# Optimization experiments

Hardware: AMD Instinct MI355X
Metric: run time of the kernel (lower is better)

## Reference

```python
import jax, jax.numpy as jnp
import numpy as np

B, T, E, H = 2, 2048, 768, 12
D = E // H  # head_dim = 64
EPS = 1e-5


def layer_norm(x, scale, shift):
    mean = x.mean(axis=-1, keepdims=True)
    # torch .var() default is unbiased (ddof=1)
    var = x.var(axis=-1, keepdims=True, ddof=1)
    return scale * (x - mean) / jnp.sqrt(var + EPS) + shift


def gelu(x):
    c = jnp.sqrt(jnp.asarray(2.0 / jnp.pi, dtype=x.dtype))
    return 0.5 * x * (1.0 + jnp.tanh(c * (x + 0.044715 * x * x * x)))


def setup_inputs() -> dict:
    key = jax.random.key(0)
    ks = jax.random.split(key, 12)
    s = 0.02
    return {
        "x": jax.random.normal(ks[0], (B, T, E), jnp.float32),
        "wq": jax.random.normal(ks[1], (E, E), jnp.float32) * s,
        "wk": jax.random.normal(ks[2], (E, E), jnp.float32) * s,
        "wv": jax.random.normal(ks[3], (E, E), jnp.float32) * s,
        "wo": jax.random.normal(ks[4], (E, E), jnp.float32) * s,
        "bo": jnp.zeros((E,), jnp.float32),
        "ln1_scale": jnp.ones((E,), jnp.float32),
        "ln1_shift": jnp.zeros((E,), jnp.float32),
        "ln2_scale": jnp.ones((E,), jnp.float32),
        "ln2_shift": jnp.zeros((E,), jnp.float32),
        "w1": jax.random.normal(ks[5], (E, 4 * E), jnp.float32) * s,
        "b1": jnp.zeros((4 * E,), jnp.float32),
        "w2": jax.random.normal(ks[6], (4 * E, E), jnp.float32) * s,
        "b2": jnp.zeros((E,), jnp.float32),
    }


def reference(x, wq, wk, wv, wo, bo, ln1_scale, ln1_shift, ln2_scale, ln2_shift,
              w1, b1, w2, b2):
    b, t, e = x.shape
    resid = x
    h = layer_norm(x, ln1_scale, ln1_shift)
    # qkv projections (no bias), split heads -> [b, H, t, D]
    q = (h @ wq).reshape(b, t, H, D).transpose(0, 2, 1, 3)
    k = (h @ wk).reshape(b, t, H, D).transpose(0, 2, 1, 3)
    v = (h @ wv).reshape(b, t, H, D).transpose(0, 2, 1, 3)
    scores = jnp.einsum("bhqd,bhkd->bhqk", q, k) / jnp.sqrt(jnp.asarray(D, x.dtype))
    causal = jnp.tril(jnp.ones((t, t), bool))
    scores = jnp.where(causal[None, None], scores, -jnp.inf)
    attn = jax.nn.softmax(scores, axis=-1)  # dropout p=0 (eval)
    ctx = jnp.einsum("bhqk,bhkd->bhqd", attn, v)
    ctx = ctx.transpose(0, 2, 1, 3).reshape(b, t, e)
    h = ctx @ wo + bo
    x = h + resid

    resid = x
    h = layer_norm(x, ln2_scale, ln2_shift)
    h = gelu(h @ w1 + b1) @ w2 + b2
    return h + resid
```

## Files before the change

### kernel.cpp

```cpp
#include <hip/hip_runtime.h>
#include <hip/hip_bf16.h>
#include <math.h>

typedef __bf16 bf16_t;
typedef __bf16 bf16x4 __attribute__((ext_vector_type(4)));
typedef __bf16 bf16x8 __attribute__((ext_vector_type(8)));
typedef float f32x4 __attribute__((ext_vector_type(4)));

#define TB 2048
#define BB 2
#define EE 768
#define HH 12
#define MM (BB * TB)
#define E3 (3 * EE)
#define E4 (4 * EE)

#define GLL16(g, l)                                                        \
  __builtin_amdgcn_global_load_lds(                                       \
      (const __attribute__((address_space(1))) void*)(g),                 \
      (__attribute__((address_space(3))) void*)(l), 16, 0, 0)

__global__ __launch_bounds__(256) void k_transpose_w(const float* __restrict__ w,
                                                     bf16_t* __restrict__ wT,
                                                     int K, int N) {
  __shared__ bf16_t tile[64][72];
  int kt = blockIdx.x * 64, nt = blockIdx.y * 64;
  int tid = threadIdx.x;
  int r = tid >> 2, c = (tid & 3) * 16;
  const float* src = w + (size_t)(kt + r) * N + nt + c;
  bf16x8 t0, t1;
#pragma unroll
  for (int j = 0; j < 8; j++) { t0[j] = (bf16_t)src[j]; t1[j] = (bf16_t)src[8 + j]; }
  *(bf16x8*)&tile[r][c] = t0;
  *(bf16x8*)&tile[r][c + 8] = t1;
  __syncthreads();
  bf16_t* dst = wT + (size_t)(nt + r) * K + kt + c;
  bf16x8 o0, o1;
#pragma unroll
  for (int j = 0; j < 8; j++) { o0[j] = tile[c + j][r]; o1[j] = tile[c + 8 + j][r]; }
  *(bf16x8*)dst = o0;
  *(bf16x8*)(dst + 8) = o1;
}

__global__ __launch_bounds__(256) void k_transpose_v(const bf16_t* __restrict__ qkv,
                                                     bf16_t* __restrict__ vt) {
  __shared__ bf16_t tile[64][72];
  int tt = blockIdx.x;
  int bh = blockIdx.y;
  int b = bh / HH, h = bh - b * HH;
  int tid = threadIdx.x;
  int r = tid >> 2, c = (tid & 3) * 16;
  const bf16_t* src = qkv + (size_t)(b * TB + tt * 64 + r) * E3 + 2 * EE + h * 64 + c;
  *(bf16x8*)&tile[r][c] = *(const bf16x8*)src;
  *(bf16x8*)&tile[r][c + 8] = *(const bf16x8*)(src + 8);
  __syncthreads();
  bf16_t* dst = vt + ((size_t)bh * 64 + r) * TB + tt * 64 + c;
  bf16x8 o0, o1;
#pragma unroll
  for (int j = 0; j < 8; j++) { o0[j] = tile[c + j][r]; o1[j] = tile[c + 8 + j][r]; }
  *(bf16x8*)dst = o0;
  *(bf16x8*)(dst + 8) = o1;
}

__global__ __launch_bounds__(256) void k_layernorm_bf16(
    const float* __restrict__ x, const float* __restrict__ sc,
    const float* __restrict__ sh, bf16_t* __restrict__ out) {
  int wave = threadIdx.x >> 6, lane = threadIdx.x & 63;
  int row = blockIdx.x * 4 + wave;
  const float* xr = x + (size_t)row * EE;
  float v[12];
  float s = 0.f, sq = 0.f;
#pragma unroll
  for (int i = 0; i < 12; i++) {
    float t = xr[lane + 64 * i];
    v[i] = t; s += t; sq += t * t;
  }
#pragma unroll
  for (int off = 1; off < 64; off <<= 1) {
    s += __shfl_xor(s, off);
    sq += __shfl_xor(sq, off);
  }
  float mean = s * (1.f / EE);
  float var = (sq - (float)EE * mean * mean) * (1.f / (EE - 1));
  float rstd = rsqrtf(var + 1e-5f);
  bf16_t* orow = out + (size_t)row * EE;
#pragma unroll
  for (int i = 0; i < 12; i++) {
    int e = lane + 64 * i;
    orow[e] = (bf16_t)(sc[e] * (v[i] - mean) * rstd + sh[e]);
  }
}

__global__ __launch_bounds__(256) void k_gemm128(
    const bf16_t* __restrict__ A, const bf16_t* __restrict__ Bt,
    int M, int N, int K, int kLen, int epi,
    float* __restrict__ outf, bf16_t* __restrict__ outb,
    const float* __restrict__ bias, const float* __restrict__ resid) {
  __shared__ bf16_t As[128 * 32];
  __shared__ bf16_t Bs[128 * 32];
  int tid = threadIdx.x;
  int wave = tid >> 6, lane = tid & 63;
  int m0 = blockIdx.y * 128, n0 = blockIdx.x * 128;
  int kOff = blockIdx.z * kLen;
  int wm = (wave >> 1) * 64, wn = (wave & 1) * 64;
  int lm = lane & 15, quad = lane >> 4;

  int srow = wave * 32 + (lane >> 2);
  int scol = (lane & 3) * 8;
  const bf16_t* Ap0 = A + (size_t)(m0 + srow) * K + kOff + scol;
  const bf16_t* Ap1 = A + (size_t)(m0 + srow + 16) * K + kOff + scol;
  const bf16_t* Bp0 = Bt + (size_t)(n0 + srow) * K + kOff + scol;
  const bf16_t* Bp1 = Bt + (size_t)(n0 + srow + 16) * K + kOff + scol;
  bf16_t* ldsA0 = &As[(wave * 32) * 32];
  bf16_t* ldsA1 = &As[(wave * 32 + 16) * 32];
  bf16_t* ldsB0 = &Bs[(wave * 32) * 32];
  bf16_t* ldsB1 = &Bs[(wave * 32 + 16) * 32];

  f32x4 acc[4][4];
#pragma unroll
  for (int i = 0; i < 4; i++)
#pragma unroll
    for (int j = 0; j < 4; j++) acc[i][j] = (f32x4){0.f, 0.f, 0.f, 0.f};

  for (int k0 = 0; k0 < kLen; k0 += 32) {
    __syncthreads();
    GLL16(Ap0 + k0, ldsA0);
    GLL16(Ap1 + k0, ldsA1);
    GLL16(Bp0 + k0, ldsB0);
    GLL16(Bp1 + k0, ldsB1);
    __syncthreads();
    bf16x8 af[4], bfr[4];
#pragma unroll
    for (int i = 0; i < 4; i++)
      af[i] = *(const bf16x8*)&As[(wm + i * 16 + lm) * 32 + quad * 8];
#pragma unroll
    for (int j = 0; j < 4; j++)
      bfr[j] = *(const bf16x8*)&Bs[(wn + j * 16 + lm) * 32 + quad * 8];
#pragma unroll
    for (int i = 0; i < 4; i++)
#pragma unroll
      for (int j = 0; j < 4; j++)
        acc[i][j] = __builtin_amdgcn_mfma_f32_16x16x32_bf16(af[i], bfr[j], acc[i][j], 0, 0, 0);
  }

  size_t pbase = (size_t)blockIdx.z * M * N;
#pragma unroll
  for (int i = 0; i < 4; i++) {
#pragma unroll
    for (int j = 0; j < 4; j++) {
      int col = n0 + wn + j * 16 + lm;
#pragma unroll
      for (int r = 0; r < 4; r++) {
        int row = m0 + wm + i * 16 + quad * 4 + r;
        size_t o = (size_t)row * N + col;
        float c = acc[i][j][r];
        if (epi == 0) {
          outb[o] = (bf16_t)c;
        } else if (epi == 1) {
          float xg = c + bias[col];
          float u = 0.7978845608028654f * (xg + 0.044715f * xg * xg * xg);
          float t = 1.f - 2.f / (__expf(2.f * u) + 1.f);
          outb[o] = (bf16_t)(0.5f * xg * (1.f + t));
        } else if (epi == 2) {
          outf[o] = c + bias[col] + resid[o];
        } else {
          outb[pbase + o] = (bf16_t)c;
        }
      }
    }
  }
}

__global__ __launch_bounds__(256) void k_reduce_ln2(
    const bf16_t* __restrict__ p, const float* __restrict__ bo_,
    const float* __restrict__ x, const float* __restrict__ sc,
    const float* __restrict__ sh, float* __restrict__ x1,
    bf16_t* __restrict__ h2) {
  int wave = threadIdx.x >> 6, lane = threadIdx.x & 63;
  int row = blockIdx.x * 4 + wave;
  const bf16_t* p0 = p + (size_t)row * EE;
  const bf16_t* p1 = p + (size_t)(MM + row) * EE;
  const float* xr = x + (size_t)row * EE;
  float v[12];
  float s = 0.f, sq = 0.f;
#pragma unroll
  for (int i = 0; i < 12; i++) {
    int e = lane + 64 * i;
    float t = (float)p0[e] + (float)p1[e] + bo_[e] + xr[e];
    v[i] = t; s += t; sq += t * t;
  }
#pragma unroll
  for (int off = 1; off < 64; off <<= 1) {
    s += __shfl_xor(s, off);
    sq += __shfl_xor(sq, off);
  }
  float mean = s * (1.f / EE);
  float var = (sq - (float)EE * mean * mean) * (1.f / (EE - 1));
  float rstd = rsqrtf(var + 1e-5f);
  float* x1r = x1 + (size_t)row * EE;
  bf16_t* h2r = h2 + (size_t)row * EE;
#pragma unroll
  for (int i = 0; i < 12; i++) {
    int e = lane + 64 * i;
    x1r[e] = v[i];
    h2r[e] = (bf16_t)(sc[e] * (v[i] - mean) * rstd + sh[e]);
  }
}

__global__ __launch_bounds__(256) void k_reduce_out(
    const bf16_t* __restrict__ p, const float* __restrict__ b2,
    const float* __restrict__ x1, float* __restrict__ out) {
  size_t e = ((size_t)blockIdx.x * 256 + threadIdx.x) * 8;
  bf16x8 a0 = *(const bf16x8*)(p + e);
  bf16x8 a1 = *(const bf16x8*)(p + (size_t)MM * EE + e);
  bf16x8 a2 = *(const bf16x8*)(p + (size_t)2 * MM * EE + e);
  bf16x8 a3 = *(const bf16x8*)(p + (size_t)3 * MM * EE + e);
  int col = (int)(e % EE);
#pragma unroll
  for (int j = 0; j < 8; j++) {
    out[e + j] = (float)a0[j] + (float)a1[j] + (float)a2[j] + (float)a3[j] +
                 b2[col + j] + x1[e + j];
  }
}

__global__ __launch_bounds__(256) void k_attn_mfma(const bf16_t* __restrict__ qkv,
                                                   const bf16_t* __restrict__ vt,
                                                   bf16_t* __restrict__ ctx) {
  __shared__ bf16_t Qs[64][72];
  __shared__ bf16_t Ks[64][72];
  __shared__ bf16_t Vt[64][72];
  __shared__ bf16_t Ps[4][16][72];

  int bh = blockIdx.x;
  int qt = 31 - blockIdx.y;
  int b = bh / HH, h = bh - b * HH;
  int q0 = qt * 64;
  int tid = threadIdx.x;
  int wave = tid >> 6, lane = tid & 63;
  int lm = lane & 15, quad = lane >> 4;
  int sr = tid >> 2, sc = (tid & 3) * 16;
  const bf16_t* vt_bh = vt + (size_t)bh * 64 * TB;

  {
    const bf16_t* src = qkv + (size_t)(b * TB + q0 + sr) * E3 + h * 64 + sc;
    bf16x8 u0 = *(const bf16x8*)src;
    bf16x8 u1 = *(const bf16x8*)(src + 8);
    bf16x8 s0, s1;
#pragma unroll
    for (int j = 0; j < 8; j++) {
      s0[j] = (bf16_t)((float)u0[j] * 0.125f);
      s1[j] = (bf16_t)((float)u1[j] * 0.125f);
    }
    *(bf16x8*)(&Qs[sr][sc]) = s0;
    *(bf16x8*)(&Qs[sr][sc + 8]) = s1;
  }
  __syncthreads();
  bf16x8 qf0 = *(const bf16x8*)(&Qs[wave * 16 + lm][quad * 8]);
  bf16x8 qf1 = *(const bf16x8*)(&Qs[wave * 16 + lm][32 + quad * 8]);

  f32x4 o_acc[4];
#pragma unroll
  for (int nt = 0; nt < 4; nt++) o_acc[nt] = (f32x4){0.f, 0.f, 0.f, 0.f};
  float m = -1e30f, l = 0.f;

  for (int kt = 0; kt <= qt; kt++) {
    __syncthreads();
    {
      const bf16_t* ksrc = qkv + (size_t)(b * TB + kt * 64 + sr) * E3 + EE + h * 64 + sc;
      *(bf16x8*)(&Ks[sr][sc]) = *(const bf16x8*)ksrc;
      *(bf16x8*)(&Ks[sr][sc + 8]) = *(const bf16x8*)(ksrc + 8);
      const bf16_t* vsrc = vt_bh + (size_t)sr * TB + kt * 64 + sc;
      *(bf16x8*)(&Vt[sr][sc]) = *(const bf16x8*)vsrc;
      *(bf16x8*)(&Vt[sr][sc + 8]) = *(const bf16x8*)(vsrc + 8);
    }
    __syncthreads();

    f32x4 st[4];
#pragma unroll
    for (int nt = 0; nt < 4; nt++) {
      st[nt] = (f32x4){0.f, 0.f, 0.f, 0.f};
      bf16x8 kf0 = *(const bf16x8*)(&Ks[nt * 16 + lm][quad * 8]);
      bf16x8 kf1 = *(const bf16x8*)(&Ks[nt * 16 + lm][32 + quad * 8]);
      st[nt] = __builtin_amdgcn_mfma_f32_16x16x32_bf16(kf0, qf0, st[nt], 0, 0, 0);
      st[nt] = __builtin_amdgcn_mfma_f32_16x16x32_bf16(kf1, qf1, st[nt], 0, 0, 0);
    }
    if (kt == qt) {
#pragma unroll
      for (int nt = 0; nt < 4; nt++)
#pragma unroll
        for (int r = 0; r < 4; r++)
          if (nt * 16 + quad * 4 + r > wave * 16 + lm) st[nt][r] = -1e30f;
    }

    float mx = -1e30f;
#pragma unroll
    for (int nt = 0; nt < 4; nt++)
#pragma unroll
      for (int r = 0; r < 4; r++) mx = fmaxf(mx, st[nt][r]);
    mx = fmaxf(mx, __shfl_xor(mx, 16));
    mx = fmaxf(mx, __shfl_xor(mx, 32));
    float mnew = fmaxf(m, mx);
    float alpha = __expf(m - mnew);
    m = mnew;

    float rs = 0.f;
#pragma unroll
    for (int nt = 0; nt < 4; nt++) {
      bf16x4 pk;
#pragma unroll
      for (int r = 0; r < 4; r++) {
        float p = __expf(st[nt][r] - m);
        pk[r] = (bf16_t)p;
        rs += p;
      }
      *(bf16x4*)(&Ps[wave][lm][nt * 16 + quad * 4]) = pk;
    }
    rs += __shfl_xor(rs, 16);
    rs += __shfl_xor(rs, 32);
    l = l * alpha + rs;

    float alpha_c[4];
#pragma unroll
    for (int r = 0; r < 4; r++) alpha_c[r] = __shfl(alpha, quad * 4 + r);
#pragma unroll
    for (int nt = 0; nt < 4; nt++)
#pragma unroll
      for (int r = 0; r < 4; r++) o_acc[nt][r] *= alpha_c[r];

    bf16x8 pf0 = *(const bf16x8*)(&Ps[wave][lm][quad * 8]);
    bf16x8 pf1 = *(const bf16x8*)(&Ps[wave][lm][32 + quad * 8]);
#pragma unroll
    for (int nt = 0; nt < 4; nt++) {
      bf16x8 vf0 = *(const bf16x8*)(&Vt[nt * 16 + lm][quad * 8]);
      bf16x8 vf1 = *(const bf16x8*)(&Vt[nt * 16 + lm][32 + quad * 8]);
      o_acc[nt] = __builtin_amdgcn_mfma_f32_16x16x32_bf16(pf0, vf0, o_acc[nt], 0, 0, 0);
      o_acc[nt] = __builtin_amdgcn_mfma_f32_16x16x32_bf16(pf1, vf1, o_acc[nt], 0, 0, 0);
    }
  }

  float inv = 1.f / l;
  float inv_c[4];
#pragma unroll
  for (int r = 0; r < 4; r++) inv_c[r] = __shfl(inv, quad * 4 + r);
#pragma unroll
  for (int nt = 0; nt < 4; nt++)
#pragma unroll
    for (int r = 0; r < 4; r++) {
      int row = q0 + wave * 16 + quad * 4 + r;
      ctx[(size_t)(b * TB + row) * EE + h * 64 + nt * 16 + lm] =
          (bf16_t)(o_acc[nt][r] * inv_c[r]);
    }
}

extern "C" void kernel_launch(void* const* d_in, const int* in_sizes, int n_in,
                              void* d_out, int out_size, void* d_ws, size_t ws_size,
                              hipStream_t stream) {
  const float* x    = (const float*)d_in[0];
  const float* wq   = (const float*)d_in[1];
  const float* wk   = (const float*)d_in[2];
  const float* wv   = (const float*)d_in[3];
  const float* wo   = (const float*)d_in[4];
  const float* bo   = (const float*)d_in[5];
  const float* ln1s = (const float*)d_in[6];
  const float* ln1b = (const float*)d_in[7];
  const float* ln2s = (const float*)d_in[8];
  const float* ln2b = (const float*)d_in[9];
  const float* w1   = (const float*)d_in[10];
  const float* b1   = (const float*)d_in[11];
  const float* w2   = (const float*)d_in[12];
  const float* b2   = (const float*)d_in[13];
  float* out = (float*)d_out;

  char* ws = (char*)d_ws;
  size_t off = 0;
  auto alloc = [&](size_t bytes) {
    char* p = ws + off;
    off += (bytes + 255) & ~(size_t)255;
    return p;
  };
  float*  x1    = (float*) alloc((size_t)MM * EE * 4);
  bf16_t* w1T   = (bf16_t*)alloc((size_t)E4 * EE * 2);
  bf16_t* w2T   = (bf16_t*)alloc((size_t)EE * E4 * 2);
  bf16_t* woT   = (bf16_t*)alloc((size_t)EE * EE * 2);
  bf16_t* wqkvT = (bf16_t*)alloc((size_t)E3 * EE * 2);
  bf16_t* hbf   = (bf16_t*)alloc((size_t)MM * EE * 2);
  bf16_t* h2    = (bf16_t*)alloc((size_t)MM * EE * 2);
  bf16_t* vtb   = (bf16_t*)alloc((size_t)BB * HH * 64 * TB * 2);
  bf16_t* part  = (bf16_t*)alloc((size_t)4 * MM * EE * 2);
  bf16_t* qkv   = (bf16_t*)alloc((size_t)MM * E3 * 2);
  bf16_t* hmid  = qkv;

  k_transpose_w<<<dim3(EE / 64, EE / 64), 256, 0, stream>>>(wq, wqkvT, EE, EE);
  k_transpose_w<<<dim3(EE / 64, EE / 64), 256, 0, stream>>>(wk, wqkvT + (size_t)EE * EE, EE, EE);
  k_transpose_w<<<dim3(EE / 64, EE / 64), 256, 0, stream>>>(wv, wqkvT + (size_t)2 * EE * EE, EE, EE);
  k_transpose_w<<<dim3(EE / 64, EE / 64), 256, 0, stream>>>(wo, woT, EE, EE);
  k_transpose_w<<<dim3(EE / 64, E4 / 64), 256, 0, stream>>>(w1, w1T, EE, E4);
  k_transpose_w<<<dim3(E4 / 64, EE / 64), 256, 0, stream>>>(w2, w2T, E4, EE);

  k_layernorm_bf16<<<MM / 4, 256, 0, stream>>>(x, ln1s, ln1b, hbf);
  k_gemm128<<<dim3(E3 / 128, MM / 128), 256, 0, stream>>>(hbf, wqkvT, MM, E3, EE, EE, 0,
                                                          nullptr, qkv, nullptr, nullptr);
  k_transpose_v<<<dim3(TB / 64, BB * HH), 256, 0, stream>>>(qkv, vtb);
  k_attn_mfma<<<dim3(BB * HH, TB / 64), 256, 0, stream>>>(qkv, vtb, hbf);
  k_gemm128<<<dim3(EE / 128, MM / 128, 2), 256, 0, stream>>>(hbf, woT, MM, EE, EE, 384, 3,
                                                             nullptr, part, nullptr, nullptr);
  k_reduce_ln2<<<MM / 4, 256, 0, stream>>>(part, bo, x, ln2s, ln2b, x1, h2);
  k_gemm128<<<dim3(E4 / 128, MM / 128), 256, 0, stream>>>(h2, w1T, MM, E4, EE, EE, 1,
                                                          nullptr, hmid, b1, nullptr);
  k_gemm128<<<dim3(EE / 128, MM / 128, 4), 256, 0, stream>>>(hmid, w2T, MM, EE, E4, E4 / 4, 3,
                                                             nullptr, part, nullptr, nullptr);
  k_reduce_out<<<(MM * EE / 8 + 255) / 256, 256, 0, stream>>>(part, b2, x1, out);
}
```

Baseline: 323.0 us.

## Double GEMM K-tile to 64 with XOR-swizzled LDS and merge weight transposes

The GEMM now stages 64-wide K slices per iteration using an XOR swizzle on LDS columns, halving barrier count and avoiding bank conflicts on fragment reads. The six weight-transpose launches are fused into one kernel that dispatches by block index. The GELU polynomial constants are pre-folded to drop a multiply. LDS use per block doubles, which may lower occupancy.

```diff
diff --git a/kernel.cpp b/kernel.cpp
--- a/kernel.cpp
+++ b/kernel.cpp
@@ -20,26 +20,46 @@
       (const __attribute__((address_space(1))) void*)(g),                 \
       (__attribute__((address_space(3))) void*)(l), 16, 0, 0)
 
-__global__ __launch_bounds__(256) void k_transpose_w(const float* __restrict__ w,
-                                                     bf16_t* __restrict__ wT,
-                                                     int K, int N) {
+__global__ __launch_bounds__(256) void k_transpose_all(
+    const float* __restrict__ wq, const float* __restrict__ wk,
+    const float* __restrict__ wv, const float* __restrict__ wo,
+    const float* __restrict__ w1, const float* __restrict__ w2,
+    bf16_t* __restrict__ wqkvT, bf16_t* __restrict__ woT,
+    bf16_t* __restrict__ w1T, bf16_t* __restrict__ w2T) {
   __shared__ bf16_t tile[64][72];
-  int kt = blockIdx.x * 64, nt = blockIdx.y * 64;
+  int id = blockIdx.x;
+  const float* src;
+  bf16_t* dst;
+  int K, N, kt, nt;
+  if (id < 576) {
+    int m = id / 144, t = id - m * 144;
+    kt = (t / 12) * 64; nt = (t % 12) * 64; K = 768; N = 768;
+    src = (m == 0) ? wq : (m == 1) ? wk : (m == 2) ? wv : wo;
+    dst = (m < 3) ? wqkvT + (size_t)m * 768 * 768 : woT;
+  } else if (id < 1152) {
+    int t = id - 576;
+    kt = (t / 48) * 64; nt = (t % 48) * 64; K = 768; N = 3072;
+    src = w1; dst = w1T;
+  } else {
+    int t = id - 1152;
+    kt = (t / 12) * 64; nt = (t % 12) * 64; K = 3072; N = 768;
+    src = w2; dst = w2T;
+  }
   int tid = threadIdx.x;
   int r = tid >> 2, c = (tid & 3) * 16;
-  const float* src = w + (size_t)(kt + r) * N + nt + c;
+  const float* s = src + (size_t)(kt + r) * N + nt + c;
   bf16x8 t0, t1;
 #pragma unroll
-  for (int j = 0; j < 8; j++) { t0[j] = (bf16_t)src[j]; t1[j] = (bf16_t)src[8 + j]; }
+  for (int j = 0; j < 8; j++) { t0[j] = (bf16_t)s[j]; t1[j] = (bf16_t)s[8 + j]; }
   *(bf16x8*)&tile[r][c] = t0;
   *(bf16x8*)&tile[r][c + 8] = t1;
   __syncthreads();
-  bf16_t* dst = wT + (size_t)(nt + r) * K + kt + c;
+  bf16_t* d = dst + (size_t)(nt + r) * K + kt + c;
   bf16x8 o0, o1;
 #pragma unroll
   for (int j = 0; j < 8; j++) { o0[j] = tile[c + j][r]; o1[j] = tile[c + 8 + j][r]; }
-  *(bf16x8*)dst = o0;
-  *(bf16x8*)(dst + 8) = o1;
+  *(bf16x8*)d = o0;
+  *(bf16x8*)(d + 8) = o1;
 }
 
 __global__ __launch_bounds__(256) void k_transpose_v(const bf16_t* __restrict__ qkv,
@@ -96,8 +116,8 @@
     int M, int N, int K, int kLen, int epi,
     float* __restrict__ outf, bf16_t* __restrict__ outb,
     const float* __restrict__ bias, const float* __restrict__ resid) {
-  __shared__ bf16_t As[128 * 32];
-  __shared__ bf16_t Bs[128 * 32];
+  __shared__ bf16_t As[128 * 64];
+  __shared__ bf16_t Bs[128 * 64];
   int tid = threadIdx.x;
   int wave = tid >> 6, lane = tid & 63;
   int m0 = blockIdx.y * 128, n0 = blockIdx.x * 128;
@@ -105,16 +125,17 @@
   int wm = (wave >> 1) * 64, wn = (wave & 1) * 64;
   int lm = lane & 15, quad = lane >> 4;
 
-  int srow = wave * 32 + (lane >> 2);
-  int scol = (lane & 3) * 8;
-  const bf16_t* Ap0 = A + (size_t)(m0 + srow) * K + kOff + scol;
-  const bf16_t* Ap1 = A + (size_t)(m0 + srow + 16) * K + kOff + scol;
-  const bf16_t* Bp0 = Bt + (size_t)(n0 + srow) * K + kOff + scol;
-  const bf16_t* Bp1 = Bt + (size_t)(n0 + srow + 16) * K + kOff + scol;
-  bf16_t* ldsA0 = &As[(wave * 32) * 32];
-  bf16_t* ldsA1 = &As[(wave * 32 + 16) * 32];
-  bf16_t* ldsB0 = &Bs[(wave * 32) * 32];
-  bf16_t* ldsB1 = &Bs[(wave * 32 + 16) * 32];
+  int srow = wave * 32 + (lane >> 3);
+  int scol = (((lane & 7) ^ ((lane >> 3) & 7)) * 8);
+  const bf16_t* Ap = A + (size_t)(m0 + srow) * K + kOff + scol;
+  const bf16_t* Bp = Bt + (size_t)(n0 + srow) * K + kOff + scol;
+  bf16_t* ldsA[4];
+  bf16_t* ldsB[4];
+#pragma unroll
+  for (int j = 0; j < 4; j++) {
+    ldsA[j] = &As[(wave * 32 + j * 8) * 64];
+    ldsB[j] = &Bs[(wave * 32 + j * 8) * 64];
+  }
 
   f32x4 acc[4][4];
 #pragma unroll
@@ -122,25 +143,33 @@
 #pragma unroll
     for (int j = 0; j < 4; j++) acc[i][j] = (f32x4){0.f, 0.f, 0.f, 0.f};
 
-  for (int k0 = 0; k0 < kLen; k0 += 32) {
+  for (int k0 = 0; k0 < kLen; k0 += 64) {
     __syncthreads();
-    GLL16(Ap0 + k0, ldsA0);
-    GLL16(Ap1 + k0, ldsA1);
-    GLL16(Bp0 + k0, ldsB0);
-    GLL16(Bp1 + k0, ldsB1);
+#pragma unroll
+    for (int j = 0; j < 4; j++) {
+      GLL16(Ap + k0 + (size_t)j * 8 * K, ldsA[j]);
+      GLL16(Bp + k0 + (size_t)j * 8 * K, ldsB[j]);
+    }
     __syncthreads();
-    bf16x8 af[4], bfr[4];
-#pragma unroll
-    for (int i = 0; i < 4; i++)
-      af[i] = *(const bf16x8*)&As[(wm + i * 16 + lm) * 32 + quad * 8];
-#pragma unroll
-    for (int j = 0; j < 4; j++)
-      bfr[j] = *(const bf16x8*)&Bs[(wn + j * 16 + lm) * 32 + quad * 8];
-#pragma unroll
-    for (int i = 0; i < 4; i++)
-#pragma unroll
-      for (int j = 0; j < 4; j++)
-        acc[i][j] = __builtin_amdgcn_mfma_f32_16x16x32_bf16(af[i], bfr[j], acc[i][j], 0, 0, 0);
+#pragma unroll
+    for (int c = 0; c < 2; c++) {
+      bf16x8 af[4], bfr[4];
+#pragma unroll
+      for (int i = 0; i < 4; i++) {
+        int r = wm + i * 16 + lm;
+        af[i] = *(const bf16x8*)&As[r * 64 + (((c * 4 + quad) ^ (lm & 7)) * 8)];
+      }
+#pragma unroll
+      for (int j = 0; j < 4; j++) {
+        int r = wn + j * 16 + lm;
+        bfr[j] = *(const bf16x8*)&Bs[r * 64 + (((c * 4 + quad) ^ (lm & 7)) * 8)];
+      }
+#pragma unroll
+      for (int i = 0; i < 4; i++)
+#pragma unroll
+        for (int j = 0; j < 4; j++)
+          acc[i][j] = __builtin_amdgcn_mfma_f32_16x16x32_bf16(af[i], bfr[j], acc[i][j], 0, 0, 0);
+    }
   }
 
   size_t pbase = (size_t)blockIdx.z * M * N;
@@ -158,8 +187,8 @@
           outb[o] = (bf16_t)c;
         } else if (epi == 1) {
           float xg = c + bias[col];
-          float u = 0.7978845608028654f * (xg + 0.044715f * xg * xg * xg);
-          float t = 1.f - 2.f / (__expf(2.f * u) + 1.f);
+          float u2 = xg * 1.5957691216057308f + xg * xg * xg * 0.07135481627561393f;
+          float t = 1.f - 2.f / (__expf(u2) + 1.f);
           outb[o] = (bf16_t)(0.5f * xg * (1.f + t));
         } else if (epi == 2) {
           outf[o] = c + bias[col] + resid[o];
@@ -390,13 +419,8 @@
   bf16_t* qkv   = (bf16_t*)alloc((size_t)MM * E3 * 2);
   bf16_t* hmid  = qkv;
 
-  k_transpose_w<<<dim3(EE / 64, EE / 64), 256, 0, stream>>>(wq, wqkvT, EE, EE);
-  k_transpose_w<<<dim3(EE / 64, EE / 64), 256, 0, stream>>>(wk, wqkvT + (size_t)EE * EE, EE, EE);
-  k_transpose_w<<<dim3(EE / 64, EE / 64), 256, 0, stream>>>(wv, wqkvT + (size_t)2 * EE * EE, EE, EE);
-  k_transpose_w<<<dim3(EE / 64, EE / 64), 256, 0, stream>>>(wo, woT, EE, EE);
-  k_transpose_w<<<dim3(EE / 64, E4 / 64), 256, 0, stream>>>(w1, w1T, EE, E4);
-  k_transpose_w<<<dim3(E4 / 64, EE / 64), 256, 0, stream>>>(w2, w2T, E4, EE);
-
+  k_transpose_all<<<1728, 256, 0, stream>>>(wq, wk, wv, wo, w1, w2,
+                                            wqkvT, woT, w1T, w2T);
   k_layernorm_bf16<<<MM / 4, 256, 0, stream>>>(x, ln1s, ln1b, hbf);
   k_gemm128<<<dim3(E3 / 128, MM / 128), 256, 0, stream>>>(hbf, wqkvT, MM, E3, EE, EE, 0,
                                                           nullptr, qkv, nullptr, nullptr);
```

Result: faster. 292.4 us (-9.5%).
